# Kernel optimization log

Measured on AMD Instinct MI355X. Metric: run time of the kernel, lower is better.

## Reference

```python
import jax, jax.numpy as jnp
import numpy as np
import math

DIMS = 2560
N_HEADS = 32
ROT_DIM = 32  # partial rotary (Phi-2)
BASE = 10000.0
B, L = 1, 2048


def apply_rope(x, rot_dim=ROT_DIM, base=BASE, offset=0):
    # x: [B, H, L, hd]; rotate first rot_dim features, pass rest through
    Lx = x.shape[2]
    D = rot_dim // 2
    pos = jnp.arange(offset, offset + Lx, dtype=jnp.float32)              # [L]
    freq = jnp.exp(-jnp.arange(D, dtype=jnp.float32) * (math.log(base) / D))  # [D]
    theta = pos[:, None] * freq[None, :]                                   # [L, D]
    cos, sin = jnp.cos(theta), jnp.sin(theta)
    x1 = x[..., :D]
    x2 = x[..., D:rot_dim]
    rx1 = x1 * cos - x2 * sin
    rx2 = x1 * sin + x2 * cos
    return jnp.concatenate([rx1, rx2, x[..., rot_dim:]], axis=-1)


def setup_inputs() -> dict:
    key = jax.random.key(0)
    k1, k2, k3, k4, k5 = jax.random.split(key, 5)
    x = jax.random.normal(k1, (B, L, DIMS), dtype=jnp.float32)
    Wqkv_w = jax.random.normal(k2, (3 * DIMS, DIMS), dtype=jnp.float32) * 0.02
    Wqkv_b = jax.random.normal(k3, (3 * DIMS,), dtype=jnp.float32) * 0.02
    out_w = jax.random.normal(k4, (DIMS, DIMS), dtype=jnp.float32) * 0.02
    out_b = jax.random.normal(k5, (DIMS,), dtype=jnp.float32) * 0.02
    # additive causal mask, broadcast over batch/heads
    mask = jnp.triu(jnp.full((L, L), -1e9, dtype=jnp.float32), k=1)[None, None]
    return {"x": x, "Wqkv_w": Wqkv_w, "Wqkv_b": Wqkv_b,
            "out_w": out_w, "out_b": out_b, "mask": mask}


def reference(x, Wqkv_w, Wqkv_b, out_w, out_b, mask):
    Bx, Lx, _ = x.shape
    hd = DIMS // N_HEADS  # 80
    qkv = x @ Wqkv_w.T + Wqkv_b                          # [B, L, 3*dims]
    q, k, v = jnp.split(qkv, 3, axis=-1)
    def to_heads(t):
        return t.reshape(Bx, Lx, N_HEADS, hd).transpose(0, 2, 1, 3)  # [B,H,L,hd]
    q, k, v = to_heads(q), to_heads(k), to_heads(v)
    q = apply_rope(q)
    k = apply_rope(k)
    scale = 1.0 / math.sqrt(hd)
    scores = scale * jnp.einsum('bhqd,bhkd->bhqk', q, k) + mask  # [B,H,L,L]
    probs = jax.nn.softmax(scores, axis=-1)
    out = jnp.einsum('bhqk,bhkd->bhqd', probs, v)
    out = out.transpose(0, 2, 1, 3).reshape(Bx, Lx, DIMS)
    return out @ out_w.T + out_b
```

## Files before the change

kernel.cpp:

```cpp
#include <hip/hip_runtime.h>
#include <cstdint>
#include <cmath>

typedef __attribute__((ext_vector_type(4))) float f32x4;
typedef __attribute__((ext_vector_type(8))) short s16x8;

#define LOG2E 1.4426950408889634f

__device__ __forceinline__ unsigned short f2bf(float f) {
    unsigned int u = __float_as_uint(f);
    u += 0x7FFFu + ((u >> 16) & 1u);
    return (unsigned short)(u >> 16);
}
__device__ __forceinline__ float bf2f(unsigned short s) {
    return __uint_as_float(((unsigned int)s) << 16);
}

__device__ __forceinline__ void async_copy16(const void* g, void* l) {
    __builtin_amdgcn_global_load_lds(
        (const __attribute__((address_space(1))) unsigned int*)(uintptr_t)g,
        (__attribute__((address_space(3))) unsigned int*)(uintptr_t)l,
        16, 0, 0);
}

__global__ __launch_bounds__(256) void cast_bf16_kernel(const float* __restrict__ in,
                                                        unsigned short* __restrict__ out,
                                                        int n4) {
    int i = blockIdx.x * 256 + threadIdx.x;
    if (i < n4) {
        float4 v = ((const float4*)in)[i];
        ushort4 o;
        o.x = f2bf(v.x); o.y = f2bf(v.y); o.z = f2bf(v.z); o.w = f2bf(v.w);
        ((ushort4*)out)[i] = o;
    }
}

template <bool BF16_OUT>
__global__ __launch_bounds__(256) void gemm_bt(const unsigned short* __restrict__ A,
                                               const unsigned short* __restrict__ B,
                                               const float* __restrict__ bias,
                                               void* __restrict__ Cout,
                                               int M, int N, int K) {
    __shared__ unsigned short As[128 * 64];
    __shared__ unsigned short Bs[128 * 64];
    const int tid  = threadIdx.x;
    const int lane = tid & 63;
    const int wv   = tid >> 6;
    const int m0 = blockIdx.y * 128;
    const int n0 = blockIdx.x * 128;
    const int w_row = (wv >> 1) * 64;
    const int w_col = (wv & 1) * 64;
    const int fr = lane & 15;
    const int fg = lane >> 4;
    const int srow = lane >> 3;
    const int scol = ((lane & 7) ^ srow) * 8;
    const int rofs0 = ((fg ^ (fr & 7))) * 8;
    const int rofs1 = rofs0 ^ 32;

    f32x4 acc[4][4];
    const f32x4 zf = {0.f, 0.f, 0.f, 0.f};
    for (int r = 0; r < 4; ++r)
        for (int c = 0; c < 4; ++c) acc[r][c] = zf;

    const unsigned short* gA = A + (size_t)(m0 + wv * 32 + srow) * K + scol;
    const unsigned short* gB = B + (size_t)(n0 + wv * 32 + srow) * K + scol;

    for (int k0 = 0; k0 < K; k0 += 64) {
        for (int i = 0; i < 4; ++i)
            async_copy16(gA + (size_t)i * 8 * K + k0, &As[(wv * 32 + i * 8) * 64]);
        for (int i = 0; i < 4; ++i)
            async_copy16(gB + (size_t)i * 8 * K + k0, &Bs[(wv * 32 + i * 8) * 64]);
        __syncthreads();
        {
            s16x8 af[4], bf[4];
            for (int r = 0; r < 4; ++r)
                af[r] = *(const s16x8*)&As[(w_row + r * 16 + fr) * 64 + rofs0];
            for (int c = 0; c < 4; ++c)
                bf[c] = *(const s16x8*)&Bs[(w_col + c * 16 + fr) * 64 + rofs0];
            for (int r = 0; r < 4; ++r)
                for (int c = 0; c < 4; ++c)
                    acc[r][c] = __builtin_amdgcn_mfma_f32_16x16x32_bf16(af[r], bf[c], acc[r][c], 0, 0, 0);
        }
        {
            s16x8 af[4], bf[4];
            for (int r = 0; r < 4; ++r)
                af[r] = *(const s16x8*)&As[(w_row + r * 16 + fr) * 64 + rofs1];
            for (int c = 0; c < 4; ++c)
                bf[c] = *(const s16x8*)&Bs[(w_col + c * 16 + fr) * 64 + rofs1];
            for (int r = 0; r < 4; ++r)
                for (int c = 0; c < 4; ++c)
                    acc[r][c] = __builtin_amdgcn_mfma_f32_16x16x32_bf16(af[r], bf[c], acc[r][c], 0, 0, 0);
        }
        __syncthreads();
    }

    const int rb = (lane >> 4) * 4;
    for (int c = 0; c < 4; ++c) {
        int col = n0 + w_col + c * 16 + fr;
        float bv = bias[col];
        for (int r = 0; r < 4; ++r) {
            int row = m0 + w_row + r * 16 + rb;
            for (int q = 0; q < 4; ++q) {
                float v = acc[r][c][q] + bv;
                if constexpr (BF16_OUT)
                    ((unsigned short*)Cout)[(size_t)(row + q) * N + col] = f2bf(v);
                else
                    ((float*)Cout)[(size_t)(row + q) * N + col] = v;
            }
        }
    }
}


#define BAR()   __builtin_amdgcn_s_barrier()
#define VMW(N)  asm volatile("s_waitcnt vmcnt(" #N ")" ::: "memory")

#define STAGE2(gXb, XsBuf, rb, kk) \
    async_copy16(gXb + (size_t)(rb) * K + (kk), (void*)&XsBuf[(rb) * 64])

#define ST_AS0(b, kk) { STAGE2(gAb, As[b], rbA_0, kk);      STAGE2(gAb, As[b], rbA_1, kk); }
#define ST_AS1(b, kk) { STAGE2(gAb, As[b], rbA_0 + 64, kk); STAGE2(gAb, As[b], rbA_1 + 64, kk); }
#define ST_BS0(b, kk) { STAGE2(gBb, Bs[b], rbB_0, kk);      STAGE2(gBb, Bs[b], rbB_1, kk); }
#define ST_BS1(b, kk) { STAGE2(gBb, Bs[b], rbB_0 + 32, kk); STAGE2(gBb, Bs[b], rbB_1 + 32, kk); }

#define READ_A(b, mh) \
    _Pragma("unroll") \
    for (int mm_ = 0; mm_ < 4; ++mm_) { \
        const unsigned short* ap_ = &As[b][(wr * 128 + (mh) * 64 + mm_ * 16 + fr) * 64]; \
        Ar[mm_][0] = *(const s16x8*)(ap_ + rofs0); \
        Ar[mm_][1] = *(const s16x8*)(ap_ + rofs1); \
    }

#define READ_B(b, nh, Brg) \
    _Pragma("unroll") \
    for (int nn_ = 0; nn_ < 2; ++nn_) { \
        const unsigned short* bp_ = &Bs[b][(wc * 64 + (nh) * 32 + nn_ * 16 + fr) * 64]; \
        Brg[nn_][0] = *(const s16x8*)(bp_ + rofs0); \
        Brg[nn_][1] = *(const s16x8*)(bp_ + rofs1); \
    }

#define MFMA_Q(mh, nh, Brg) \
    _Pragma("unroll") \
    for (int mm_ = 0; mm_ < 4; ++mm_) { \
        _Pragma("unroll") \
        for (int nn_ = 0; nn_ < 2; ++nn_) { \
            acc[(mh) * 4 + mm_][(nh) * 2 + nn_] = __builtin_amdgcn_mfma_f32_16x16x32_bf16( \
                Ar[mm_][0], Brg[nn_][0], acc[(mh) * 4 + mm_][(nh) * 2 + nn_], 0, 0, 0); \
            acc[(mh) * 4 + mm_][(nh) * 2 + nn_] = __builtin_amdgcn_mfma_f32_16x16x32_bf16( \
                Ar[mm_][1], Brg[nn_][1], acc[(mh) * 4 + mm_][(nh) * 2 + nn_], 0, 0, 0); \
        } \
    }

#define GROUP(b, t) { \
    int x1_ = (t) + 1; if (x1_ >= ktiles) x1_ -= ktiles; \
    int x2_ = (t) + 2; if (x2_ >= ktiles) x2_ -= ktiles; \
    const int kn1 = x1_ << 6; \
    const int kn2 = x2_ << 6; \
     \
    __builtin_amdgcn_s_setprio(1); MFMA_Q(0, 0, Br0); __builtin_amdgcn_s_setprio(0); \
    VMW(6); \
    READ_B(b, 1, Br1); \
    ST_AS1((b) ^ 1, kn1); \
    BAR(); \
     \
    __builtin_amdgcn_s_setprio(1); MFMA_Q(0, 1, Br1); __builtin_amdgcn_s_setprio(0); \
    VMW(6); \
    READ_A(b, 1); \
    ST_AS0(b, kn2); \
    BAR(); \
     \
    __builtin_amdgcn_s_setprio(1); MFMA_Q(1, 1, Br1); __builtin_amdgcn_s_setprio(0); \
    VMW(6); \
    ST_BS0(b, kn2); \
    BAR(); \
     \
    __builtin_amdgcn_s_setprio(1); MFMA_Q(1, 0, Br0); __builtin_amdgcn_s_setprio(0); \
    VMW(6); \
    READ_A((b) ^ 1, 0); \
    READ_B((b) ^ 1, 0, Br0); \
    ST_BS1(b, kn2); \
    BAR(); \
}

__global__ __launch_bounds__(512, 2) void gemm256_bt(const unsigned short* __restrict__ A,
                                                     const unsigned short* __restrict__ B,
                                                     const float* __restrict__ bias,
                                                     unsigned short* __restrict__ C,
                                                     int M, int N, int K) {
    __shared__ unsigned short As[2][256 * 64];
    __shared__ unsigned short Bs[2][256 * 64];
    const int tid  = threadIdx.x;
    const int lane = tid & 63;
    const int wv   = tid >> 6;
    const int wr   = wv >> 2;
    const int wc   = wv & 3;
    const int j     = blockIdx.x & 7;
    const int local = blockIdx.x >> 3;
    const int strip = 2 * (j & 3) + (local & 1);
    const int panel = (j >> 2) * 15 + (local >> 1);
    const int m0 = strip * 256;
    const int n0 = panel * 256;
    const int fr = lane & 15;
    const int fg = lane >> 4;
    const int rofs0 = (fg ^ (fr & 7)) * 8;
    const int rofs1 = rofs0 ^ 32;
    const int rlane = lane >> 3;
    const int swzc  = ((lane & 7) ^ (rlane & 7)) * 8;
    const int idx0 = wv * 2, idx1 = wv * 2 + 1;
    const int rbA_0 = idx0 * 8 + ((idx0 >= 8) ? 64 : 0);
    const int rbA_1 = idx1 * 8 + ((idx1 >= 8) ? 64 : 0);
    const int rbB_0 = (idx0 >> 2) * 64 + (idx0 & 3) * 8;
    const int rbB_1 = (idx1 >> 2) * 64 + (idx1 & 3) * 8;
    const int ktiles = K >> 6;

    const unsigned short* gAb = A + (size_t)(m0 + rlane) * K + swzc;
    const unsigned short* gBb = B + (size_t)(n0 + rlane) * K + swzc;

    f32x4 acc[8][4];
    const f32x4 zf = {0.f, 0.f, 0.f, 0.f};
#pragma unroll
    for (int i = 0; i < 8; ++i)
#pragma unroll
        for (int jj = 0; jj < 4; ++jj) acc[i][jj] = zf;

    s16x8 Ar[4][2], Br0[2][2], Br1[2][2];

    ST_AS0(0, 0); ST_AS1(0, 0); ST_BS0(0, 0); ST_BS1(0, 0);
    ST_AS0(1, 64); ST_BS0(1, 64); ST_BS1(1, 64);
    VMW(6);
    BAR();
    READ_A(0, 0);
    READ_B(0, 0, Br0);

    const int nit = ktiles >> 1;
    for (int it = 0; it < nit; ++it) {
        GROUP(0, it * 2);
        GROUP(1, it * 2 + 1);
    }

    const int rb = (lane >> 4) * 4;
#pragma unroll
    for (int nn = 0; nn < 4; ++nn) {
        int col = n0 + wc * 64 + nn * 16 + fr;
        float bv = bias[col];
#pragma unroll
        for (int mm = 0; mm < 8; ++mm) {
            int row = m0 + wr * 128 + mm * 16 + rb;
#pragma unroll
            for (int q = 0; q < 4; ++q) {
                float v = acc[mm][nn][q] + bv;
                C[(size_t)(row + q) * N + col] = f2bf(v);
            }
        }
    }
}

__global__ __launch_bounds__(256) void rope_q_kernel(unsigned short* __restrict__ qkv) {
    int g = blockIdx.x * 256 + threadIdx.x;
    int c = g & 1;
    int h = (g >> 1) & 31;
    int p = g >> 6;
    size_t base = (size_t)p * 7680 + h * 80 + c * 8;
    s16x8 x1v = *(const s16x8*)(qkv + base);
    s16x8 x2v = *(const s16x8*)(qkv + base + 16);
    s16x8 o1, o2;
    for (int j = 0; j < 8; ++j) {
        int dp = c * 8 + j;
        float freq = expf(-(float)dp * 0.57564627324851142f);
        float sn, cs;
        sincosf((float)p * freq, &sn, &cs);
        float x1 = bf2f((unsigned short)x1v[j]);
        float x2 = bf2f((unsigned short)x2v[j]);
        o1[j] = (short)f2bf(x1 * cs - x2 * sn);
        o2[j] = (short)f2bf(x1 * sn + x2 * cs);
    }
    *(s16x8*)(qkv + base)      = o1;
    *(s16x8*)(qkv + base + 16) = o2;
}

__global__ __launch_bounds__(256) void rope_pack_k_kernel(const unsigned short* __restrict__ qkv,
                                                          unsigned short* __restrict__ Kp) {
    int g = blockIdx.x * 256 + threadIdx.x;
    int c   = g % 12;
    int h   = (g / 12) & 31;
    int pos = g / 384;
    int d0 = c * 8;
    const unsigned short* kb = qkv + (size_t)pos * 7680 + 2560 + h * 80;
    s16x8 v = {0, 0, 0, 0, 0, 0, 0, 0};
    if (c >= 4) {
        if (d0 < 80) v = *(const s16x8*)(kb + d0);
    } else if (c < 2) {
        s16x8 x1v = *(const s16x8*)(kb + d0);
        s16x8 x2v = *(const s16x8*)(kb + d0 + 16);
        for (int j = 0; j < 8; ++j) {
            int dp = d0 + j;
            float freq = expf(-(float)dp * 0.57564627324851142f);
            float sn, cs;
            sincosf((float)pos * freq, &sn, &cs);
            v[j] = (short)f2bf(bf2f((unsigned short)x1v[j]) * cs -
                               bf2f((unsigned short)x2v[j]) * sn);
        }
    } else {
        s16x8 x1v = *(const s16x8*)(kb + d0 - 16);
        s16x8 x2v = *(const s16x8*)(kb + d0);
        for (int j = 0; j < 8; ++j) {
            int dp = d0 - 16 + j;
            float freq = expf(-(float)dp * 0.57564627324851142f);
            float sn, cs;
            sincosf((float)pos * freq, &sn, &cs);
            v[j] = (short)f2bf(bf2f((unsigned short)x1v[j]) * sn +
                               bf2f((unsigned short)x2v[j]) * cs);
        }
    }
    *(s16x8*)(Kp + ((size_t)h * 2048 + pos) * 96 + d0) = v;
}

__global__ __launch_bounds__(256) void pack_v_kernel(const unsigned short* __restrict__ qkv,
                                                     unsigned short* __restrict__ Vp) {
    int h  = blockIdx.x & 31;
    int g64 = blockIdx.x >> 5;
    int k0 = g64 * 64;
    int tid = threadIdx.x;
    for (int ci = tid; ci < 320; ci += 256) {
        int d   = ci % 80;
        int kbl = ci / 80;
        unsigned short tmp[16];
        for (int j = 0; j < 16; ++j)
            tmp[j] = qkv[(size_t)(k0 + kbl * 16 + j) * 7680 + 5120 + h * 80 + d];
        unsigned short* dst = Vp + ((size_t)h * 128 + g64 * 4 + kbl) * 1280 + d * 16;
        *(s16x8*)dst       = *(const s16x8*)&tmp[0];
        *(s16x8*)(dst + 8) = *(const s16x8*)&tmp[8];
    }
}

__global__ __launch_bounds__(256) void flash3_kernel(const unsigned short* __restrict__ qkv,
                                                     const unsigned short* __restrict__ Kp,
                                                     const unsigned short* __restrict__ Vp,
                                                     unsigned short* __restrict__ attn) {
    __shared__ unsigned short Pt[4][640];
    __shared__ float parts[2][16][84];
    __shared__ float parts_l[2][16];
    const int tid  = threadIdx.x;
    const int lane = tid & 63;
    const int wv   = tid >> 6;
    const int h = blockIdx.x & 31;
    const int p = blockIdx.x >> 5;
    const int s    = (wv < 2) ? p : (127 - p);
    const int j    = wv & 1;
    const int slot = wv >> 1;
    const int fr = lane & 15;
    const int fg = lane >> 4;
    const float k1 = 0.11180339887498949f * LOG2E;
    const int sm16 = s * 16;

    const int n    = s + 1;
    const int half = (n + 1) >> 1;
    const int kstart = (j ? half : 0) * 16;
    const int kend   = (j ? n : half) * 16;

    s16x8 qf[3];
    {
        const unsigned short* qb = qkv + (size_t)(sm16 + fr) * 7680 + h * 80;
        const s16x8 zs = {0, 0, 0, 0, 0, 0, 0, 0};
        for (int sd = 0; sd < 3; ++sd) {
            int d = 32 * sd + fg * 8;
            qf[sd] = (d < 80) ? *(const s16x8*)(qb + d) : zs;
        }
    }

    f32x4 O[5];
    const f32x4 zf = {0.f, 0.f, 0.f, 0.f};
    for (int t = 0; t < 5; ++t) O[t] = zf;
    float rs[4] = {0.f, 0.f, 0.f, 0.f};

    const unsigned short* kptr = Kp + (size_t)h * 2048 * 96 + (size_t)(kstart + fr) * 96 + fg * 8;
    const unsigned short* vptr = Vp + (size_t)h * 128 * 1280 + (size_t)(kstart >> 4) * 1280
                                 + (fg >> 1) * 1280 + fr * 16 + (fg & 1) * 8;
    unsigned short* Pw = &Pt[wv][0];

#define LOADK(KB) { \
    _Pragma("unroll") \
    for (int g = 0; g < 2; ++g) \
        _Pragma("unroll") \
        for (int sd = 0; sd < 3; ++sd) \
            KB[g][sd] = *(const s16x8*)(kptr + g * 1536 + sd * 32); \
    kptr += 3072; }

#define FSTEP(KB, k0v) { \
    s16x8 vb[5]; \
    _Pragma("unroll") \
    for (int t = 0; t < 5; ++t) vb[t] = *(const s16x8*)(vptr + t * 256); \
    vptr += 2560; \
    f32x4 sa[2] = {zf, zf}; \
    __builtin_amdgcn_s_setprio(1); \
    _Pragma("unroll") \
    for (int g = 0; g < 2; ++g) \
        _Pragma("unroll") \
        for (int sd = 0; sd < 3; ++sd) \
            sa[g] = __builtin_amdgcn_mfma_f32_16x16x32_bf16(qf[sd], KB[g][sd], sa[g], 0, 0, 0); \
    __builtin_amdgcn_s_setprio(0); \
    if ((k0v) + 32 > sm16 || (k0v) + 32 > kend) { \
        _Pragma("unroll") \
        for (int g = 0; g < 2; ++g) \
            _Pragma("unroll") \
            for (int r = 0; r < 4; ++r) { \
                int key  = (k0v) + g * 16 + fr; \
                int qrow = sm16 + fg * 4 + r; \
                if (key > qrow || key >= kend) sa[g][r] = -1e30f; \
            } \
    } \
    float pr[2][4]; \
    _Pragma("unroll") \
    for (int g = 0; g < 2; ++g) \
        _Pragma("unroll") \
        for (int r = 0; r < 4; ++r) \
            pr[g][r] = __builtin_amdgcn_exp2f(sa[g][r] * k1); \
    _Pragma("unroll") \
    for (int r = 0; r < 4; ++r) rs[r] += pr[0][r] + pr[1][r]; \
    _Pragma("unroll") \
    for (int g = 0; g < 2; ++g) \
        _Pragma("unroll") \
        for (int r = 0; r < 4; ++r) \
            Pw[(fg * 4 + r) * 40 + g * 16 + fr] = \
                (unsigned short)(__float_as_uint(pr[g][r]) >> 16); \
    s16x8 pa = *(const s16x8*)(Pw + fr * 40 + fg * 8); \
    __builtin_amdgcn_s_setprio(1); \
    _Pragma("unroll") \
    for (int t = 0; t < 5; ++t) \
        O[t] = __builtin_amdgcn_mfma_f32_16x16x32_bf16(pa, vb[t], O[t], 0, 0, 0); \
    __builtin_amdgcn_s_setprio(0); }

    s16x8 kbA[2][3], kbB[2][3];
    int nst = (kend - kstart + 31) >> 5;
    int k0  = kstart;
    if (nst > 0) {
        LOADK(kbA);
        while (true) {
            if (nst >= 2) LOADK(kbB);
            FSTEP(kbA, k0);
            k0 += 32;
            if (nst <= 1) break;
            if (nst >= 3) LOADK(kbA);
            FSTEP(kbB, k0);
            k0 += 32;
            if (nst <= 2) break;
            nst -= 2;
        }
    }
#undef LOADK
#undef FSTEP

    for (int r = 0; r < 4; ++r) {
        float v = rs[r];
        v += __shfl_xor(v, 1);
        v += __shfl_xor(v, 2);
        v += __shfl_xor(v, 4);
        v += __shfl_xor(v, 8);
        rs[r] = v;
    }

    if (j) {
        for (int t = 0; t < 5; ++t)
            for (int r = 0; r < 4; ++r)
                parts[slot][fg * 4 + r][t * 16 + fr] = O[t][r];
        if (fr == 0)
            for (int r = 0; r < 4; ++r) parts_l[slot][fg * 4 + r] = rs[r];
    }
    __syncthreads();
    if (!j) {
        for (int r = 0; r < 4; ++r) {
            float rl = 1.0f / (rs[r] + parts_l[slot][fg * 4 + r]);
            int row = sm16 + fg * 4 + r;
            for (int t = 0; t < 5; ++t) {
                float v = (O[t][r] + parts[slot][fg * 4 + r][t * 16 + fr]) * rl;
                attn[(size_t)row * 2560 + h * 80 + t * 16 + fr] = f2bf(v);
            }
        }
    }
}

extern "C" void kernel_launch(void* const* d_in, const int* in_sizes, int n_in,
                              void* d_out, int out_size, void* d_ws, size_t ws_size,
                              hipStream_t stream) {
    const float* x    = (const float*)d_in[0];
    const float* wqkv = (const float*)d_in[1];
    const float* bqkv = (const float*)d_in[2];
    const float* outw = (const float*)d_in[3];
    const float* outb = (const float*)d_in[4];

    unsigned short* xb    = (unsigned short*)d_ws;
    unsigned short* wqkvb = xb + (size_t)2048 * 2560;
    unsigned short* Kp    = wqkvb;
    unsigned short* Vp    = wqkvb + (size_t)32 * 2048 * 96;
    unsigned short* outwb = wqkvb + (size_t)7680 * 2560;
    unsigned short* qkvb  = outwb + (size_t)2560 * 2560;
    unsigned short* attnb = qkvb  + (size_t)2048 * 7680;
    float* out = (float*)d_out;

    cast_bf16_kernel<<<2048 * 2560 / 4 / 256, 256, 0, stream>>>(x, xb, 2048 * 2560 / 4);
    cast_bf16_kernel<<<7680 * 2560 / 4 / 256, 256, 0, stream>>>(wqkv, wqkvb, 7680 * 2560 / 4);
    cast_bf16_kernel<<<2560 * 2560 / 4 / 256, 256, 0, stream>>>(outw, outwb, 2560 * 2560 / 4);

    gemm256_bt<<<240, 512, 0, stream>>>(xb, wqkvb, bqkv, qkvb, 2048, 7680, 2560);

    rope_q_kernel<<<2048 * 64 / 256, 256, 0, stream>>>(qkvb);
    rope_pack_k_kernel<<<2048 * 384 / 256, 256, 0, stream>>>(qkvb, Kp);
    pack_v_kernel<<<32 * 32, 256, 0, stream>>>(qkvb, Vp);

    flash3_kernel<<<2048, 256, 0, stream>>>(qkvb, Kp, Vp, attnb);

    gemm_bt<false><<<dim3(2560 / 128, 2048 / 128), 256, 0, stream>>>(
        attnb, outwb, outb, (void*)out, 2048, 2560, 2560);
}
```

Measured before the change: 426.3 us.

## Share K/V tiles across waves via async LDS staging in flash attention

The attention kernel is restructured so each block handles one head and eight query tiles (two per wave, paired to balance causal work). K and V tiles are staged into double-buffered LDS with async global-to-LDS copies and shared by all four waves, instead of each wave loading them from global memory. The K pack layout is changed to match the LDS tile layout. This removes the split-K partial merge and cuts redundant global traffic, but runs 4x fewer blocks (512) and adds a per-iteration block barrier, so waves doing less causal work wait on the others.

```diff
diff --git a/kernel.cpp b/kernel.cpp
--- a/kernel.cpp
+++ b/kernel.cpp
@@ -312,7 +312,7 @@
                                bf2f((unsigned short)x2v[j]) * cs);
         }
     }
-    *(s16x8*)(Kp + ((size_t)h * 2048 + pos) * 96 + d0) = v;
+    *(s16x8*)(Kp + (((size_t)h * 64 + (pos >> 5)) * 12 + c) * 256 + (pos & 31) * 8) = v;
 }
 
 __global__ __launch_bounds__(256) void pack_v_kernel(const unsigned short* __restrict__ qkv,
@@ -333,80 +333,82 @@
     }
 }
 
-__global__ __launch_bounds__(256) void flash3_kernel(const unsigned short* __restrict__ qkv,
+__global__ __launch_bounds__(256) void flash6_kernel(const unsigned short* __restrict__ qkv,
                                                      const unsigned short* __restrict__ Kp,
                                                      const unsigned short* __restrict__ Vp,
                                                      unsigned short* __restrict__ attn) {
+    __shared__ unsigned short Ks[2][3072];
+    __shared__ unsigned short Vs[2][2560];
     __shared__ unsigned short Pt[4][640];
-    __shared__ float parts[2][16][84];
-    __shared__ float parts_l[2][16];
     const int tid  = threadIdx.x;
     const int lane = tid & 63;
     const int wv   = tid >> 6;
-    const int h = blockIdx.x & 31;
-    const int p = blockIdx.x >> 5;
-    const int s    = (wv < 2) ? p : (127 - p);
-    const int j    = wv & 1;
-    const int slot = wv >> 1;
+    const int h  = blockIdx.x & 31;
+    const int jj = blockIdx.x >> 5;
     const int fr = lane & 15;
     const int fg = lane >> 4;
     const float k1 = 0.11180339887498949f * LOG2E;
-    const int sm16 = s * 16;
-
-    const int n    = s + 1;
-    const int half = (n + 1) >> 1;
-    const int kstart = (j ? half : 0) * 16;
-    const int kend   = (j ? n : half) * 16;
-
-    s16x8 qf[3];
+
+    const int sA  = jj + 16 * wv;
+    const int sB  = jj + 112 - 16 * wv;
+    const int smA = sA * 16;
+    const int smB = sB * 16;
+    const int Ublk = (jj + 114) >> 1;
+
+    const s16x8 zs = {0, 0, 0, 0, 0, 0, 0, 0};
+    s16x8 qfA[3], qfB[3];
     {
-        const unsigned short* qb = qkv + (size_t)(sm16 + fr) * 7680 + h * 80;
-        const s16x8 zs = {0, 0, 0, 0, 0, 0, 0, 0};
+        const unsigned short* qa = qkv + (size_t)(smA + fr) * 7680 + h * 80;
+        const unsigned short* qb = qkv + (size_t)(smB + fr) * 7680 + h * 80;
         for (int sd = 0; sd < 3; ++sd) {
             int d = 32 * sd + fg * 8;
-            qf[sd] = (d < 80) ? *(const s16x8*)(qb + d) : zs;
-        }
-    }
-
-    f32x4 O[5];
+            qfA[sd] = (d < 80) ? *(const s16x8*)(qa + d) : zs;
+            qfB[sd] = (d < 80) ? *(const s16x8*)(qb + d) : zs;
+        }
+    }
+
+    f32x4 OA[5], OB[5];
     const f32x4 zf = {0.f, 0.f, 0.f, 0.f};
-    for (int t = 0; t < 5; ++t) O[t] = zf;
-    float rs[4] = {0.f, 0.f, 0.f, 0.f};
-
-    const unsigned short* kptr = Kp + (size_t)h * 2048 * 96 + (size_t)(kstart + fr) * 96 + fg * 8;
-    const unsigned short* vptr = Vp + (size_t)h * 128 * 1280 + (size_t)(kstart >> 4) * 1280
-                                 + (fg >> 1) * 1280 + fr * 16 + (fg & 1) * 8;
+    for (int t = 0; t < 5; ++t) { OA[t] = zf; OB[t] = zf; }
+    float rsA[4] = {0.f, 0.f, 0.f, 0.f};
+    float rsB[4] = {0.f, 0.f, 0.f, 0.f};
     unsigned short* Pw = &Pt[wv][0];
 
-#define LOADK(KB) { \
+    const unsigned short* Kh = Kp + (size_t)h * 196608;
+    const unsigned short* Vh = Vp + (size_t)h * 163840;
+
+#define STG1(q, b, uu) { \
+    if ((q) < 6) async_copy16(Kh + (size_t)(uu) * 3072 + (q) * 512 + lane * 8, &Ks[b][(q) * 512]); \
+    else         async_copy16(Vh + (size_t)(uu) * 2560 + ((q) - 6) * 512 + lane * 8, &Vs[b][((q) - 6) * 512]); }
+#define STAGEU(b, uu) { STG1(wv, b, uu); STG1(wv + 4, b, uu); if (wv < 3) STG1(wv + 8, b, uu); }
+
+#define FSTEP6(QF, OO, RS, SM16, K0, BUF) { \
+    s16x8 kb[2][3]; \
     _Pragma("unroll") \
     for (int g = 0; g < 2; ++g) \
         _Pragma("unroll") \
         for (int sd = 0; sd < 3; ++sd) \
-            KB[g][sd] = *(const s16x8*)(kptr + g * 1536 + sd * 32); \
-    kptr += 3072; }
-
-#define FSTEP(KB, k0v) { \
+            kb[g][sd] = *(const s16x8*)&Ks[BUF][(fg + sd * 4) * 256 + (g * 16 + fr) * 8]; \
     s16x8 vb[5]; \
     _Pragma("unroll") \
-    for (int t = 0; t < 5; ++t) vb[t] = *(const s16x8*)(vptr + t * 256); \
-    vptr += 2560; \
+    for (int t = 0; t < 5; ++t) \
+        vb[t] = *(const s16x8*)&Vs[BUF][(fg >> 1) * 1280 + t * 256 + fr * 16 + (fg & 1) * 8]; \
     f32x4 sa[2] = {zf, zf}; \
     __builtin_amdgcn_s_setprio(1); \
     _Pragma("unroll") \
     for (int g = 0; g < 2; ++g) \
         _Pragma("unroll") \
         for (int sd = 0; sd < 3; ++sd) \
-            sa[g] = __builtin_amdgcn_mfma_f32_16x16x32_bf16(qf[sd], KB[g][sd], sa[g], 0, 0, 0); \
+            sa[g] = __builtin_amdgcn_mfma_f32_16x16x32_bf16(QF[sd], kb[g][sd], sa[g], 0, 0, 0); \
     __builtin_amdgcn_s_setprio(0); \
-    if ((k0v) + 32 > sm16 || (k0v) + 32 > kend) { \
+    if ((K0) + 32 > (SM16)) { \
         _Pragma("unroll") \
         for (int g = 0; g < 2; ++g) \
             _Pragma("unroll") \
             for (int r = 0; r < 4; ++r) { \
-                int key  = (k0v) + g * 16 + fr; \
-                int qrow = sm16 + fg * 4 + r; \
-                if (key > qrow || key >= kend) sa[g][r] = -1e30f; \
+                int key  = (K0) + g * 16 + fr; \
+                int qrow = (SM16) + fg * 4 + r; \
+                if (key > qrow) sa[g][r] = -1e30f; \
             } \
     } \
     float pr[2][4]; \
@@ -416,7 +418,7 @@
         for (int r = 0; r < 4; ++r) \
             pr[g][r] = __builtin_amdgcn_exp2f(sa[g][r] * k1); \
     _Pragma("unroll") \
-    for (int r = 0; r < 4; ++r) rs[r] += pr[0][r] + pr[1][r]; \
+    for (int r = 0; r < 4; ++r) RS[r] += pr[0][r] + pr[1][r]; \
     _Pragma("unroll") \
     for (int g = 0; g < 2; ++g) \
         _Pragma("unroll") \
@@ -427,56 +429,45 @@
     __builtin_amdgcn_s_setprio(1); \
     _Pragma("unroll") \
     for (int t = 0; t < 5; ++t) \
-        O[t] = __builtin_amdgcn_mfma_f32_16x16x32_bf16(pa, vb[t], O[t], 0, 0, 0); \
+        OO[t] = __builtin_amdgcn_mfma_f32_16x16x32_bf16(pa, vb[t], OO[t], 0, 0, 0); \
     __builtin_amdgcn_s_setprio(0); }
 
-    s16x8 kbA[2][3], kbB[2][3];
-    int nst = (kend - kstart + 31) >> 5;
-    int k0  = kstart;
-    if (nst > 0) {
-        LOADK(kbA);
-        while (true) {
-            if (nst >= 2) LOADK(kbB);
-            FSTEP(kbA, k0);
-            k0 += 32;
-            if (nst <= 1) break;
-            if (nst >= 3) LOADK(kbA);
-            FSTEP(kbB, k0);
-            k0 += 32;
-            if (nst <= 2) break;
-            nst -= 2;
-        }
-    }
-#undef LOADK
-#undef FSTEP
-
-    for (int r = 0; r < 4; ++r) {
-        float v = rs[r];
-        v += __shfl_xor(v, 1);
-        v += __shfl_xor(v, 2);
-        v += __shfl_xor(v, 4);
-        v += __shfl_xor(v, 8);
-        rs[r] = v;
-    }
-
-    if (j) {
-        for (int t = 0; t < 5; ++t)
-            for (int r = 0; r < 4; ++r)
-                parts[slot][fg * 4 + r][t * 16 + fr] = O[t][r];
-        if (fr == 0)
-            for (int r = 0; r < 4; ++r) parts_l[slot][fg * 4 + r] = rs[r];
-    }
+    STAGEU(0, 0);
     __syncthreads();
-    if (!j) {
-        for (int r = 0; r < 4; ++r) {
-            float rl = 1.0f / (rs[r] + parts_l[slot][fg * 4 + r]);
-            int row = sm16 + fg * 4 + r;
-            for (int t = 0; t < 5; ++t) {
-                float v = (O[t][r] + parts[slot][fg * 4 + r][t * 16 + fr]) * rl;
-                attn[(size_t)row * 2560 + h * 80 + t * 16 + fr] = f2bf(v);
-            }
-        }
-    }
+    int buf = 0;
+    for (int u = 0; u < Ublk; ++u) {
+        if (u + 1 < Ublk) STAGEU(buf ^ 1, u + 1);
+        const int k0 = u * 32;
+        if (2 * u <= sA) FSTEP6(qfA, OA, rsA, smA, k0, buf);
+        if (2 * u <= sB) FSTEP6(qfB, OB, rsB, smB, k0, buf);
+        __syncthreads();
+        buf ^= 1;
+    }
+#undef STG1
+#undef STAGEU
+#undef FSTEP6
+
+#define FIN6(RS, OO, SM16) { \
+    _Pragma("unroll") \
+    for (int r = 0; r < 4; ++r) { \
+        float v = RS[r]; \
+        v += __shfl_xor(v, 1); \
+        v += __shfl_xor(v, 2); \
+        v += __shfl_xor(v, 4); \
+        v += __shfl_xor(v, 8); \
+        RS[r] = v; \
+    } \
+    _Pragma("unroll") \
+    for (int r = 0; r < 4; ++r) { \
+        float rl = 1.0f / RS[r]; \
+        int row = (SM16) + fg * 4 + r; \
+        _Pragma("unroll") \
+        for (int t = 0; t < 5; ++t) \
+            attn[(size_t)row * 2560 + h * 80 + t * 16 + fr] = f2bf(OO[t][r] * rl); \
+    } }
+    FIN6(rsA, OA, smA);
+    FIN6(rsB, OB, smB);
+#undef FIN6
 }
 
 extern "C" void kernel_launch(void* const* d_in, const int* in_sizes, int n_in,
@@ -507,7 +498,7 @@
     rope_pack_k_kernel<<<2048 * 384 / 256, 256, 0, stream>>>(qkvb, Kp);
     pack_v_kernel<<<32 * 32, 256, 0, stream>>>(qkvb, Vp);
 
-    flash3_kernel<<<2048, 256, 0, stream>>>(qkvb, Kp, Vp, attnb);
+    flash6_kernel<<<512, 256, 0, stream>>>(qkvb, Kp, Vp, attnb);
 
     gemm_bt<false><<<dim3(2560 / 128, 2048 / 128), 256, 0, stream>>>(
         attnb, outwb, outb, (void*)out, 2048, 2560, 2560);
```

After: 416.0 us. 1.02x faster.
